# Kernel optimization log

Measured on AMD Instinct MI355X. Metric: run time of the kernel, lower is better.

## Reference

```python
import jax, jax.numpy as jnp
import numpy as np

C_IN, CH, HCH, NFFT, HOP, NL, K = 100, 512, 1536, 1024, 256, 8, 4
B, T = 16, 1024

def conv1d(x, w, b=None, pad=0, groups=1):
    # x: [B, Cin, L], w: [Cout, Cin/groups, K]
    y = jax.lax.conv_general_dilated(x, w, (1,), [(pad, pad)],
        dimension_numbers=('NCH', 'OIH', 'NCH'), feature_group_count=groups)
    if b is not None:
        y = y + b[None, :, None]
    return y

def layernorm(x, g, b, eps=1e-5):
    # normalize over last axis (channel), torch LayerNorm semantics (biased var)
    mu = jnp.mean(x, -1, keepdims=True)
    var = jnp.var(x, -1, keepdims=True)
    return (x - mu) * jax.lax.rsqrt(var + eps) * g + b

def setup_inputs() -> dict:
    key = jax.random.key(0)
    ks = jax.random.split(key, 8)
    r = lambda k, s: jax.random.normal(k, s, jnp.float32) * 0.02
    return {
        'x': jax.random.normal(ks[0], (B, C_IN, T), jnp.float32),
        'in_w': r(ks[1], (CH, C_IN, 7)), 'in_b': jnp.zeros((CH,), jnp.float32),
        'norm_g': jnp.ones((CH,), jnp.float32), 'norm_b': jnp.zeros((CH,), jnp.float32),
        'dw_w': r(ks[2], (NL, CH, 1, 7)), 'dw_b': jnp.zeros((NL, CH), jnp.float32),
        'ln_g': jnp.ones((NL, CH), jnp.float32), 'ln_b': jnp.zeros((NL, CH), jnp.float32),
        'pw1_w': r(ks[3], (NL, HCH, CH)), 'pw1_b': jnp.zeros((NL, HCH), jnp.float32),
        'pw2_w': r(ks[4], (NL, CH, HCH)), 'pw2_b': jnp.zeros((NL, CH), jnp.float32),
        'ls': jnp.full((NL, CH), 1.0 / NL, jnp.float32),
        'normL_g': jnp.ones((CH,), jnp.float32), 'normL_b': jnp.zeros((CH,), jnp.float32),
        'out_w': r(ks[5], (NFFT, CH, 1)), 'out_b': jnp.zeros((NFFT,), jnp.float32),
        'ov_w': r(ks[6], (HOP, NFFT, K)),
    }

def reference(x, in_w, in_b, norm_g, norm_b, dw_w, dw_b, ln_g, ln_b,
              pw1_w, pw1_b, pw2_w, pw2_b, ls, normL_g, normL_b, out_w, out_b, ov_w):
    x = conv1d(x, in_w, in_b, pad=3)                                   # [B, CH, T]
    x = layernorm(x.transpose(0, 2, 1), norm_g, norm_b).transpose(0, 2, 1)

    def layer(h, p):
        dw, db, g, b, w1, b1, w2, b2, s = p
        y = conv1d(h, dw, db, pad=3, groups=CH)                        # depthwise 7-tap
        y = layernorm(y.transpose(0, 2, 1), g, b)                      # [B, T, CH]
        y = jnp.einsum('btc,hc->bth', y, w1) + b1                      # pointwise expand
        y = jax.nn.gelu(y, approximate=False)
        y = jnp.einsum('bth,ch->btc', y, w2) + b2                      # pointwise project
        return h + (y * s).transpose(0, 2, 1), None

    x, _ = jax.lax.scan(layer, x, (dw_w, dw_b, ln_g, ln_b, pw1_w, pw1_b, pw2_w, pw2_b, ls))
    x = layernorm(x.transpose(0, 2, 1), normL_g, normL_b).transpose(0, 2, 1)
    o = conv1d(x, out_w, out_b, pad=0)                                 # [B, NFFT, T]
    # --- overlap_add ---
    o = conv1d(o, ov_w, None, pad=K - 1)                               # [B, HOP, L], L = T + K - 1
    Bn, C, L = o.shape
    pad_size = C * K - L + K - 1
    o = jnp.pad(o, ((0, 0), (0, 0), (0, pad_size)))
    idx = (jnp.arange(L)[None, :] + jnp.arange(C)[:, None] * (C * K - 1)) % L  # [C, L]
    o = jnp.take_along_axis(o, jnp.broadcast_to(idx[None], (Bn, C, L)), axis=2)
    o = jnp.sum(o, axis=1, keepdims=True)                              # [B, 1, L]
    return o[..., K // 2 : L - K // 2 + 1]                             # [B, 1, T]
```

## Files before the change

kernel.cpp:

```cpp
#include <hip/hip_runtime.h>

#define B_    16
#define CIN   100
#define T_    1024
#define CH_   512
#define HCH_  1536
#define NL_   8
#define NFFT_ 1024
#define HOP_  256
#define BT    (B_ * T_)
#define L_    1027
#define OROWS 1032
#define KIN   704

typedef __bf16 bf16x8 __attribute__((ext_vector_type(8)));
typedef float f32x4 __attribute__((ext_vector_type(4)));
typedef short s16x8 __attribute__((ext_vector_type(8)));

__device__ __forceinline__ short f2b(float f) {
  unsigned u = __float_as_uint(f);
  u += 0x7fffu + ((u >> 16) & 1u);
  return (short)(u >> 16);
}
__device__ __forceinline__ float b2f(short s) {
  return __uint_as_float(((unsigned)(unsigned short)s) << 16);
}

__device__ __forceinline__ void gl2lds16(const void* g, void* l) {
  __builtin_amdgcn_global_load_lds(
      (__attribute__((address_space(1))) void*)g,
      (__attribute__((address_space(3))) void*)l, 16, 0, 0);
}

__global__ __launch_bounds__(256) void k_cvt(const float* __restrict__ s,
                                             short* __restrict__ d, int n) {
  for (int i = blockIdx.x * 256 + threadIdx.x; i < n; i += gridDim.x * 256)
    d[i] = f2b(s[i]);
}

__global__ __launch_bounds__(256) void k_cvt_ov(const float* __restrict__ w,
                                                short* __restrict__ d) {
  const int n = 4 * HOP_ * NFFT_;
  for (int i = blockIdx.x * 256 + threadIdx.x; i < n; i += gridDim.x * 256) {
    int k = i >> 18;
    int rem = i & 0x3FFFF;
    int c = rem >> 10, nn = rem & 1023;
    d[i] = f2b(w[((size_t)c * NFFT_ + nn) * 4 + k]);
  }
}

__global__ __launch_bounds__(256) void k_cvt_inw(const float* __restrict__ w,
                                                 short* __restrict__ d) {
  const int n = CH_ * KIN;
  for (int i = blockIdx.x * 256 + threadIdx.x; i < n; i += gridDim.x * 256) {
    int c = i / KIN, e = i - c * KIN;
    d[i] = (e < 700) ? f2b(w[c * 700 + e]) : (short)0;
  }
}

__global__ __launch_bounds__(256) void k_cvt_dwt(const float* __restrict__ w,
                                                 float* __restrict__ d) {
  const int n = NL_ * 7 * CH_;
  for (int i = blockIdx.x * 256 + threadIdx.x; i < n; i += gridDim.x * 256) {
    int l = i / (7 * CH_), r = i - l * 7 * CH_;
    int k = r >> 9, c = r & 511;
    d[i] = w[((size_t)l * CH_ + c) * 7 + k];
  }
}

__global__ __launch_bounds__(256) void k_im2col(const float* __restrict__ x,
                                                short* __restrict__ xim) {
  const int total = BT * KIN;
  for (int i = blockIdx.x * 256 + threadIdx.x; i < total; i += gridDim.x * 256) {
    int m = i / KIN, e = i - m * KIN;
    int b = m >> 10, t = m & 1023;
    int ci = e / 7, k = e - ci * 7;
    int tt = t + k - 3;
    float v = (e < 700 && tt >= 0 && tt < T_) ? x[((b * CIN + ci) << 10) + tt] : 0.f;
    xim[i] = f2b(v);
  }
}

__global__ __launch_bounds__(256) void k_zeropad(short* __restrict__ o1p) {
  int i = blockIdx.x * 256 + threadIdx.x;
  int b = i >> 13;
  int r8 = (i >> 10) & 7;
  int nn = i & 1023;
  int row = r8 < 4 ? r8 : (OROWS - 8 + r8);
  o1p[((size_t)b * OROWS + row) * NFFT_ + nn] = 0;
}

__global__ __launch_bounds__(256) void k_lnb(const short* __restrict__ in,
                                             short* __restrict__ outp,
                                             const float* __restrict__ g,
                                             const float* __restrict__ bta) {
  int row = blockIdx.x, tid = threadIdx.x;
  unsigned u = *reinterpret_cast<const unsigned*>(&in[(size_t)row * CH_ + tid * 2]);
  float v0 = __uint_as_float(u << 16);
  float v1 = __uint_as_float(u & 0xffff0000u);
  float s = v0 + v1, q = v0 * v0 + v1 * v1;
#pragma unroll
  for (int o = 32; o > 0; o >>= 1) { s += __shfl_down(s, o); q += __shfl_down(q, o); }
  __shared__ float sh[8];
  int wid = tid >> 6, lane = tid & 63;
  if (lane == 0) { sh[wid] = s; sh[wid + 4] = q; }
  __syncthreads();
  float S = sh[0] + sh[1] + sh[2] + sh[3];
  float Q = sh[4] + sh[5] + sh[6] + sh[7];
  float mu  = S * (1.f / 512.f);
  float var = Q * (1.f / 512.f) - mu * mu;
  float r = rsqrtf(var + 1e-5f);
  float x0 = (v0 - mu) * r * g[tid * 2]     + bta[tid * 2];
  float x1 = (v1 - mu) * r * g[tid * 2 + 1] + bta[tid * 2 + 1];
  unsigned o = ((unsigned)(unsigned short)f2b(x0)) |
               (((unsigned)(unsigned short)f2b(x1)) << 16);
  *reinterpret_cast<unsigned*>(&outp[(size_t)row * CH_ + tid * 2]) = o;
}

__global__ __launch_bounds__(256) void k_dwln(const short* __restrict__ h,
                                              const float* __restrict__ dwt,
                                              const float* __restrict__ dwb,
                                              const float* __restrict__ g,
                                              const float* __restrict__ bta,
                                              short* __restrict__ yb) {
  int b = blockIdx.x, t0 = blockIdx.y * 32;
  int tid = threadIdx.x, lane = tid & 63, w = tid >> 6;
  __shared__ short hs[38][512];
  for (int e = tid; e < 38 * 64; e += 256) {
    int row = e >> 6, seg = (e & 63) << 3;
    int t = t0 - 3 + row;
    s16x8 v = {};
    if (t >= 0 && t < T_)
      v = *reinterpret_cast<const s16x8*>(&h[((size_t)((b << 10) + t)) * CH_ + seg]);
    *reinterpret_cast<s16x8*>(&hs[row][seg]) = v;
  }
  const int c0 = lane << 3;
  float wk[7][8];
#pragma unroll
  for (int k = 0; k < 7; ++k) {
    f32x4 lo = *reinterpret_cast<const f32x4*>(&dwt[k * CH_ + c0]);
    f32x4 hi = *reinterpret_cast<const f32x4*>(&dwt[k * CH_ + c0 + 4]);
#pragma unroll
    for (int j = 0; j < 4; ++j) { wk[k][j] = lo[j]; wk[k][j + 4] = hi[j]; }
  }
  float bb[8], gg[8], be[8];
  {
    f32x4 a = *reinterpret_cast<const f32x4*>(&dwb[c0]);
    f32x4 b4 = *reinterpret_cast<const f32x4*>(&dwb[c0 + 4]);
    f32x4 c = *reinterpret_cast<const f32x4*>(&g[c0]);
    f32x4 d = *reinterpret_cast<const f32x4*>(&g[c0 + 4]);
    f32x4 e = *reinterpret_cast<const f32x4*>(&bta[c0]);
    f32x4 f = *reinterpret_cast<const f32x4*>(&bta[c0 + 4]);
#pragma unroll
    for (int j = 0; j < 4; ++j) {
      bb[j] = a[j]; bb[j + 4] = b4[j];
      gg[j] = c[j]; gg[j + 4] = d[j];
      be[j] = e[j]; be[j + 4] = f[j];
    }
  }
  __syncthreads();
#pragma unroll
  for (int i = 0; i < 8; ++i) {
    int r = w * 8 + i;
    float acc[8];
#pragma unroll
    for (int j = 0; j < 8; ++j) acc[j] = bb[j];
#pragma unroll
    for (int k = 0; k < 7; ++k) {
      s16x8 hv = *reinterpret_cast<const s16x8*>(&hs[r + k][c0]);
#pragma unroll
      for (int j = 0; j < 8; ++j) acc[j] += b2f(hv[j]) * wk[k][j];
    }
    float s = 0.f, q = 0.f;
#pragma unroll
    for (int j = 0; j < 8; ++j) { s += acc[j]; q += acc[j] * acc[j]; }
#pragma unroll
    for (int o = 32; o > 0; o >>= 1) { s += __shfl_xor(s, o); q += __shfl_xor(q, o); }
    float mu  = s * (1.f / 512.f);
    float var = q * (1.f / 512.f) - mu * mu;
    float rr = rsqrtf(var + 1e-5f);
    s16x8 ov;
#pragma unroll
    for (int j = 0; j < 8; ++j) ov[j] = f2b((acc[j] - mu) * rr * gg[j] + be[j]);
    *reinterpret_cast<s16x8*>(&yb[((size_t)((b << 10) + t0 + r)) * CH_ + c0]) = ov;
  }
}

template <int MODE>
__global__ __launch_bounds__(256) void k_mgemm(const short* __restrict__ A,
                                               const short* __restrict__ Bw,
                                               const float* __restrict__ bias,
                                               const float* __restrict__ scale,
                                               short* __restrict__ obf,
                                               int N, int K) {
  __shared__ __align__(16) short As[128 * 64];
  __shared__ __align__(16) short Bs[128 * 64];
  const int tid = threadIdx.x;
  const int lane = tid & 63, w = tid >> 6;
  const int id = blockIdx.x;
  const int ny = N >> 7;
  const int g8 = id >> 3;
  const int gq = g8 / ny;
  const int mt = (id & 7) + (gq << 3);
  const int nt = g8 - gq * ny;
  const int m0 = mt << 7, n0 = nt << 7;
  const int wr = (w >> 1) * 64, wc = (w & 1) * 64;
  f32x4 acc[4][4];
#pragma unroll
  for (int i = 0; i < 4; ++i)
#pragma unroll
    for (int j = 0; j < 4; ++j) acc[i][j] = (f32x4){0.f, 0.f, 0.f, 0.f};

  const short* Ab = A + (size_t)m0 * K;
  const short* Bb = Bw + (size_t)n0 * K;
  int r_[4], kk_[4];
#pragma unroll
  for (int j = 0; j < 4; ++j) {
    int c = tid + j * 256;
    r_[j] = c >> 3;
    kk_[j] = (((c & 7) ^ (r_[j] & 7)) * 8);
  }
  short* AsB[4]; short* BsB[4];
#pragma unroll
  for (int j = 0; j < 4; ++j) {
    AsB[j] = As + (j * 256 + w * 64) * 8;
    BsB[j] = Bs + (j * 256 + w * 64) * 8;
  }
  const int ar = wr + (lane & 15);
  const int br = wc + (lane & 15);
  const int hi = lane >> 4;

  for (int k0 = 0; k0 < K; k0 += 64) {
#pragma unroll
    for (int j = 0; j < 4; ++j) gl2lds16(Ab + (size_t)r_[j] * K + k0 + kk_[j], AsB[j]);
#pragma unroll
    for (int j = 0; j < 4; ++j) gl2lds16(Bb + (size_t)r_[j] * K + k0 + kk_[j], BsB[j]);
    asm volatile("s_waitcnt vmcnt(0)" ::: "memory");
    __syncthreads();
#pragma unroll
    for (int ks = 0; ks < 2; ++ks) {
      bf16x8 a[4], b[4];
#pragma unroll
      for (int f = 0; f < 4; ++f) {
        int row = ar + f * 16;
        a[f] = *reinterpret_cast<const bf16x8*>(&As[row * 64 + (((ks * 4 + hi) ^ (row & 7)) * 8)]);
      }
#pragma unroll
      for (int f = 0; f < 4; ++f) {
        int row = br + f * 16;
        b[f] = *reinterpret_cast<const bf16x8*>(&Bs[row * 64 + (((ks * 4 + hi) ^ (row & 7)) * 8)]);
      }
#pragma unroll
      for (int fi = 0; fi < 4; ++fi)
#pragma unroll
        for (int fj = 0; fj < 4; ++fj)
          acc[fi][fj] = __builtin_amdgcn_mfma_f32_16x16x32_bf16(a[fi], b[fj], acc[fi][fj], 0, 0, 0);
    }
    __syncthreads();
  }
  const int mb = m0 + wr + (hi << 2);
  const int nb = n0 + wc + (lane & 15);
#pragma unroll
  for (int fj = 0; fj < 4; ++fj) {
    int n = nb + fj * 16;
    float bi = bias[n];
    float sc = (MODE == 2) ? scale[n] : 0.f;
#pragma unroll
    for (int fi = 0; fi < 4; ++fi) {
      int mrow = mb + fi * 16;
#pragma unroll
      for (int r = 0; r < 4; ++r) {
        float v = acc[fi][fj][r] + bi;
        int m = mrow + r;
        if (MODE == 0) {
          obf[(size_t)m * N + n] = f2b(v);
        } else if (MODE == 1) {
          v = 0.5f * v * (1.f + erff(v * 0.70710678118654752440f));
          obf[(size_t)m * N + n] = f2b(v);
        } else if (MODE == 2) {
          size_t idx = (size_t)m * N + n;
          obf[idx] = f2b(b2f(obf[idx]) + v * sc);
        } else {
          int bb = m >> 10, t = m & 1023;
          obf[((size_t)(bb * OROWS + 4 + t)) * NFFT_ + n] = f2b(v);
        }
      }
    }
  }
}

__global__ __launch_bounds__(256) void k_ovgemm(const short* __restrict__ o1p,
                                                const short* __restrict__ ovb,
                                                float* __restrict__ o2) {
  __shared__ __align__(16) short As[128 * 64];
  __shared__ __align__(16) short Bs[128 * 64];
  const int tid = threadIdx.x;
  const int lane = tid & 63, w = tid >> 6;
  const int l0 = blockIdx.x * 128, c0 = blockIdx.y * 128, b = blockIdx.z;
  const int wr = (w >> 1) * 64, wc = (w & 1) * 64;
  f32x4 acc[4][4];
#pragma unroll
  for (int i = 0; i < 4; ++i)
#pragma unroll
    for (int j = 0; j < 4; ++j) acc[i][j] = (f32x4){0.f, 0.f, 0.f, 0.f};

  const short* Ab = o1p + (size_t)b * OROWS * NFFT_;
  int r_[4], kk_[4];
#pragma unroll
  for (int j = 0; j < 4; ++j) {
    int c = tid + j * 256;
    r_[j] = c >> 3;
    kk_[j] = (((c & 7) ^ (r_[j] & 7)) * 8);
  }
  short* AsB[4]; short* BsB[4];
#pragma unroll
  for (int j = 0; j < 4; ++j) {
    AsB[j] = As + (j * 256 + w * 64) * 8;
    BsB[j] = Bs + (j * 256 + w * 64) * 8;
  }
  const int ar = wr + (lane & 15);
  const int br = wc + (lane & 15);
  const int hi = lane >> 4;

  for (int ksh = 0; ksh < 4; ++ksh) {
    const short* Bb = ovb + ((size_t)(ksh * HOP_ + c0)) * NFFT_;
    for (int k0 = 0; k0 < NFFT_; k0 += 64) {
#pragma unroll
      for (int j = 0; j < 4; ++j) {
        int tp = l0 + r_[j] + 1 + ksh;
        tp = tp > (OROWS - 1) ? (OROWS - 1) : tp;
        gl2lds16(Ab + (size_t)tp * NFFT_ + k0 + kk_[j], AsB[j]);
      }
#pragma unroll
      for (int j = 0; j < 4; ++j) gl2lds16(Bb + (size_t)r_[j] * NFFT_ + k0 + kk_[j], BsB[j]);
      asm volatile("s_waitcnt vmcnt(0)" ::: "memory");
      __syncthreads();
#pragma unroll
      for (int ks = 0; ks < 2; ++ks) {
        bf16x8 a[4], bfr[4];
#pragma unroll
        for (int f = 0; f < 4; ++f) {
          int row = ar + f * 16;
          a[f] = *reinterpret_cast<const bf16x8*>(&As[row * 64 + (((ks * 4 + hi) ^ (row & 7)) * 8)]);
        }
#pragma unroll
        for (int f = 0; f < 4; ++f) {
          int row = br + f * 16;
          bfr[f] = *reinterpret_cast<const bf16x8*>(&Bs[row * 64 + (((ks * 4 + hi) ^ (row & 7)) * 8)]);
        }
#pragma unroll
        for (int fi = 0; fi < 4; ++fi)
#pragma unroll
          for (int fj = 0; fj < 4; ++fj)
            acc[fi][fj] = __builtin_amdgcn_mfma_f32_16x16x32_bf16(a[fi], bfr[fj], acc[fi][fj], 0, 0, 0);
      }
      __syncthreads();
    }
  }
  const int lb = l0 + wr + (hi << 2);
  const int cb = c0 + wc + (lane & 15);
#pragma unroll
  for (int fj = 0; fj < 4; ++fj) {
    int c = cb + fj * 16;
#pragma unroll
    for (int fi = 0; fi < 4; ++fi) {
#pragma unroll
      for (int r = 0; r < 4; ++r) {
        int l = lb + fi * 16 + r;
        if (l < L_) o2[((size_t)b * L_ + l) * HOP_ + c] = acc[fi][fj][r];
      }
    }
  }
}

__global__ __launch_bounds__(256) void k_oadd(const float* __restrict__ o2,
                                              float* __restrict__ out) {
  int b = blockIdx.x;
  int t = blockIdx.y * 256 + threadIdx.x;
  int m = t + 2;
  float s = 0.f;
  for (int c = 0; c < HOP_; ++c) {
    s += o2[((size_t)b * L_ + m) * HOP_ + c];
    m -= 4;
    if (m < 0) m += L_;
  }
  out[b * T_ + t] = s;
}

extern "C" void kernel_launch(void* const* d_in, const int* in_sizes, int n_in,
                              void* d_out, int out_size, void* d_ws, size_t ws_size,
                              hipStream_t stream) {
  const float* x      = (const float*)d_in[0];
  const float* in_w   = (const float*)d_in[1];
  const float* in_b   = (const float*)d_in[2];
  const float* norm_g = (const float*)d_in[3];
  const float* norm_b = (const float*)d_in[4];
  const float* dw_w   = (const float*)d_in[5];
  const float* dw_b   = (const float*)d_in[6];
  const float* ln_g   = (const float*)d_in[7];
  const float* ln_b   = (const float*)d_in[8];
  const float* pw1_w  = (const float*)d_in[9];
  const float* pw1_b  = (const float*)d_in[10];
  const float* pw2_w  = (const float*)d_in[11];
  const float* pw2_b  = (const float*)d_in[12];
  const float* ls     = (const float*)d_in[13];
  const float* normLg = (const float*)d_in[14];
  const float* normLb = (const float*)d_in[15];
  const float* out_w  = (const float*)d_in[16];
  const float* out_b  = (const float*)d_in[17];
  const float* ov_w   = (const float*)d_in[18];
  float* out = (float*)d_out;

  char* p = (char*)d_ws;
  short* hb   = (short*)p; p += (size_t)BT * CH_ * 2;
  short* yb   = (short*)p; p += (size_t)BT * CH_ * 2;
  short* zb   = (short*)p; p += (size_t)BT * HCH_ * 2;
  short* pw1b = (short*)p; p += (size_t)NL_ * HCH_ * CH_ * 2;
  short* pw2b = (short*)p; p += (size_t)NL_ * CH_ * HCH_ * 2;
  short* owb  = (short*)p; p += (size_t)NFFT_ * CH_ * 2;
  short* ovb  = (short*)p; p += (size_t)4 * HOP_ * NFFT_ * 2;
  float* dwt  = (float*)p; p += (size_t)NL_ * 7 * CH_ * 4;
  short* xim  = zb;
  short* wib  = zb + (size_t)BT * KIN;
  short* hbL  = yb;
  short* o1p  = zb;
  float* o2   = (float*)hb;

  k_cvt<<<4096, 256, 0, stream>>>(pw1_w, pw1b, NL_ * HCH_ * CH_);
  k_cvt<<<4096, 256, 0, stream>>>(pw2_w, pw2b, NL_ * CH_ * HCH_);
  k_cvt<<<2048, 256, 0, stream>>>(out_w, owb, NFFT_ * CH_);
  k_cvt_ov<<<4096, 256, 0, stream>>>(ov_w, ovb);
  k_cvt_inw<<<1408, 256, 0, stream>>>(in_w, wib);
  k_cvt_dwt<<<112, 256, 0, stream>>>(dw_w, dwt);
  k_im2col<<<8192, 256, 0, stream>>>(x, xim);

  k_mgemm<0><<<512, 256, 0, stream>>>(xim, wib, in_b, nullptr, hb, CH_, KIN);
  k_lnb<<<BT, 256, 0, stream>>>(hb, hb, norm_g, norm_b);
  for (int l = 0; l < NL_; ++l) {
    k_dwln<<<dim3(B_, T_ / 32), 256, 0, stream>>>(
        hb, dwt + (size_t)l * 7 * CH_, dw_b + l * CH_,
        ln_g + l * CH_, ln_b + l * CH_, yb);
    k_mgemm<1><<<1536, 256, 0, stream>>>(
        yb, pw1b + (size_t)l * HCH_ * CH_, pw1_b + l * HCH_, nullptr, zb,
        HCH_, CH_);
    k_mgemm<2><<<512, 256, 0, stream>>>(
        zb, pw2b + (size_t)l * CH_ * HCH_, pw2_b + l * CH_, ls + l * CH_, hb,
        CH_, HCH_);
  }
  k_lnb<<<BT, 256, 0, stream>>>(hb, hbL, normLg, normLb);
  k_mgemm<3><<<1024, 256, 0, stream>>>(hbL, owb, out_b, nullptr, o1p, NFFT_, CH_);
  k_zeropad<<<512, 256, 0, stream>>>(o1p);
  k_ovgemm<<<dim3(9, 2, 16), 256, 0, stream>>>(o1p, ovb, o2);
  k_oadd<<<dim3(B_, 4), 256, 0, stream>>>(o2, out);
}
```

Measured before the change: 1.044 ms.

## Stage GEMM epilogue through LDS for vector stores; reuse A tile across overlap shifts

The mgemm epilogue now writes the bias-added (and GELU or scaled) results into shared memory with a swizzle, then each thread writes 8 contiguous bf16 values to global memory, replacing scattered 2-byte stores. For the residual mode, the read-modify-write also becomes vectorised. The ovgemm kernel loads a 136-row A tile once per k-chunk and reuses it for all four shifts by offsetting the row index, instead of reloading A for each shift. This cuts global traffic and store inefficiency, at the cost of extra LDS, an extra barrier, and a reordered loop nest.

```diff
diff --git a/kernel.cpp b/kernel.cpp
--- a/kernel.cpp
+++ b/kernel.cpp
@@ -193,8 +193,9 @@
                                                const float* __restrict__ scale,
                                                short* __restrict__ obf,
                                                int N, int K) {
-  __shared__ __align__(16) short As[128 * 64];
-  __shared__ __align__(16) short Bs[128 * 64];
+  __shared__ __align__(16) short smem[2 * 128 * 64];
+  short* As = smem;
+  short* Bs = smem + 128 * 64;
   const int tid = threadIdx.x;
   const int lane = tid & 63, w = tid >> 6;
   const int id = blockIdx.x;
@@ -258,33 +259,45 @@
     }
     __syncthreads();
   }
-  const int mb = m0 + wr + (hi << 2);
-  const int nb = n0 + wc + (lane & 15);
+  short* Cl = smem;
+  const int colbase = wc + (lane & 15);
 #pragma unroll
   for (int fj = 0; fj < 4; ++fj) {
-    int n = nb + fj * 16;
+    int cl = colbase + fj * 16;
+    int n = n0 + cl;
     float bi = bias[n];
     float sc = (MODE == 2) ? scale[n] : 0.f;
 #pragma unroll
     for (int fi = 0; fi < 4; ++fi) {
-      int mrow = mb + fi * 16;
 #pragma unroll
       for (int r = 0; r < 4; ++r) {
+        int rl = wr + (hi << 2) + fi * 16 + r;
         float v = acc[fi][fj][r] + bi;
-        int m = mrow + r;
-        if (MODE == 0) {
-          obf[(size_t)m * N + n] = f2b(v);
-        } else if (MODE == 1) {
-          v = 0.5f * v * (1.f + erff(v * 0.70710678118654752440f));
-          obf[(size_t)m * N + n] = f2b(v);
-        } else if (MODE == 2) {
-          size_t idx = (size_t)m * N + n;
-          obf[idx] = f2b(b2f(obf[idx]) + v * sc);
-        } else {
-          int bb = m >> 10, t = m & 1023;
-          obf[((size_t)(bb * OROWS + 4 + t)) * NFFT_ + n] = f2b(v);
-        }
-      }
+        if (MODE == 1) v = 0.5f * v * (1.f + erff(v * 0.70710678118654752440f));
+        if (MODE == 2) v *= sc;
+        Cl[rl * 128 + (cl ^ (((rl >> 2) & 3) << 4))] = f2b(v);
+      }
+    }
+  }
+  __syncthreads();
+  const int cs = (lane & 15) * 8;
+#pragma unroll
+  for (int it = 0; it < 8; ++it) {
+    int rl = w * 32 + it * 4 + (lane >> 4);
+    s16x8 v = *reinterpret_cast<const s16x8*>(&Cl[rl * 128 + (cs ^ (((rl >> 2) & 3) << 4))]);
+    int m = m0 + rl;
+    if (MODE == 2) {
+      size_t idx = (size_t)m * N + n0 + cs;
+      s16x8 hv = *reinterpret_cast<const s16x8*>(&obf[idx]);
+      s16x8 o;
+#pragma unroll
+      for (int j = 0; j < 8; ++j) o[j] = f2b(b2f(hv[j]) + b2f(v[j]));
+      *reinterpret_cast<s16x8*>(&obf[idx]) = o;
+    } else if (MODE == 3) {
+      int bb = m >> 10, t = m & 1023;
+      *reinterpret_cast<s16x8*>(&obf[((size_t)(bb * OROWS + 4 + t)) * NFFT_ + n0 + cs]) = v;
+    } else {
+      *reinterpret_cast<s16x8*>(&obf[(size_t)m * N + n0 + cs]) = v;
     }
   }
 }
@@ -292,7 +305,7 @@
 __global__ __launch_bounds__(256) void k_ovgemm(const short* __restrict__ o1p,
                                                 const short* __restrict__ ovb,
                                                 float* __restrict__ o2) {
-  __shared__ __align__(16) short As[128 * 64];
+  __shared__ __align__(16) short As[136 * 64];
   __shared__ __align__(16) short Bs[128 * 64];
   const int tid = threadIdx.x;
   const int lane = tid & 63, w = tid >> 6;
@@ -305,34 +318,30 @@
     for (int j = 0; j < 4; ++j) acc[i][j] = (f32x4){0.f, 0.f, 0.f, 0.f};
 
   const short* Ab = o1p + (size_t)b * OROWS * NFFT_;
-  int r_[4], kk_[4];
-#pragma unroll
-  for (int j = 0; j < 4; ++j) {
-    int c = tid + j * 256;
-    r_[j] = c >> 3;
-    kk_[j] = (((c & 7) ^ (r_[j] & 7)) * 8);
-  }
-  short* AsB[4]; short* BsB[4];
-#pragma unroll
-  for (int j = 0; j < 4; ++j) {
-    AsB[j] = As + (j * 256 + w * 64) * 8;
-    BsB[j] = Bs + (j * 256 + w * 64) * 8;
-  }
   const int ar = wr + (lane & 15);
   const int br = wc + (lane & 15);
   const int hi = lane >> 4;
-
-  for (int ksh = 0; ksh < 4; ++ksh) {
-    const short* Bb = ovb + ((size_t)(ksh * HOP_ + c0)) * NFFT_;
-    for (int k0 = 0; k0 < NFFT_; k0 += 64) {
-#pragma unroll
-      for (int j = 0; j < 4; ++j) {
-        int tp = l0 + r_[j] + 1 + ksh;
-        tp = tp > (OROWS - 1) ? (OROWS - 1) : tp;
-        gl2lds16(Ab + (size_t)tp * NFFT_ + k0 + kk_[j], AsB[j]);
-      }
-#pragma unroll
-      for (int j = 0; j < 4; ++j) gl2lds16(Bb + (size_t)r_[j] * NFFT_ + k0 + kk_[j], BsB[j]);
+  const int sl_row = lane >> 3;
+  const int sl_j   = lane & 7;
+
+  for (int k0 = 0; k0 < NFFT_; k0 += 64) {
+    for (int c = w; c < 17; c += 4) {
+      int lr = c * 8 + sl_row;
+      int gr = l0 + 1 + lr;
+      if (gr > OROWS - 1) gr = OROWS - 1;
+      int j = sl_j ^ (lr & 7);
+      gl2lds16(Ab + (size_t)gr * NFFT_ + k0 + j * 8, As + c * 512);
+    }
+#pragma unroll
+    for (int ksh = 0; ksh < 4; ++ksh) {
+      const short* Bb = ovb + ((size_t)(ksh * HOP_ + c0)) * NFFT_;
+#pragma unroll
+      for (int c = 0; c < 4; ++c) {
+        int ch = w * 4 + c;
+        int lr = ch * 8 + sl_row;
+        int j = sl_j ^ (lr & 7);
+        gl2lds16(Bb + (size_t)lr * NFFT_ + k0 + j * 8, Bs + ch * 512);
+      }
       asm volatile("s_waitcnt vmcnt(0)" ::: "memory");
       __syncthreads();
 #pragma unroll
@@ -340,7 +349,7 @@
         bf16x8 a[4], bfr[4];
 #pragma unroll
         for (int f = 0; f < 4; ++f) {
-          int row = ar + f * 16;
+          int row = ar + f * 16 + ksh;
           a[f] = *reinterpret_cast<const bf16x8*>(&As[row * 64 + (((ks * 4 + hi) ^ (row & 7)) * 8)]);
         }
 #pragma unroll
```

Measured after the change: 978.5 us. 1.07x faster.
